# Performance work log

Measured on AMD Instinct MI355X. Metric: run time of the kernel, lower is better.

The kernel has to match this reference:

```python
import jax, jax.numpy as jnp
import numpy as np

H = 2048        # hidden_size
NH = 16         # num query heads
NKV = 4         # num kv heads
HD = 128        # head_dim
EPS = 1e-6
SCALE = HD ** -0.5
GROUPS = NH // NKV


def rotate_half(x):
    x1, x2 = x[..., : HD // 2], x[..., HD // 2:]
    return jnp.concatenate((-x2, x1), axis=-1)


def rmsnorm(x, w):
    # x: [..., HD]
    var = jnp.mean(jnp.square(x), axis=-1, keepdims=True)
    return x * jax.lax.rsqrt(var + EPS) * w


def setup_inputs() -> dict:
    key = jax.random.key(0)
    ks = jax.random.split(key, 10)
    B, QL, CL = 4, 1024, 3072
    s = 0.02
    return {
        "noise": jax.random.normal(ks[0], (B, QL, H), jnp.float32),
        "ctx": jax.random.normal(ks[1], (B, CL, H), jnp.float32),
        "cos": jax.random.uniform(ks[2], (B, CL + QL, HD), jnp.float32, -1.0, 1.0),
        "sin": jax.random.uniform(ks[3], (B, CL + QL, HD), jnp.float32, -1.0, 1.0),
        "Wq": jax.random.normal(ks[4], (H, NH * HD), jnp.float32) * s,
        "Wk": jax.random.normal(ks[5], (H, NKV * HD), jnp.float32) * s,
        "Wv": jax.random.normal(ks[6], (H, NKV * HD), jnp.float32) * s,
        "Wo": jax.random.normal(ks[7], (NH * HD, H), jnp.float32) * s,
        "qn_w": jnp.ones((HD,), jnp.float32),
        "kn_w": jnp.ones((HD,), jnp.float32),
    }


def reference(noise, ctx, cos, sin, Wq, Wk, Wv, Wo, qn_w, kn_w):
    B, QL, _ = noise.shape
    CL = ctx.shape[1]
    KL = CL + QL

    # Q from noise
    q = (noise @ Wq).reshape(B, QL, NH, HD)
    q = rmsnorm(q, qn_w).transpose(0, 2, 1, 3)            # [B, NH, QL, HD]

    # K/V from [ctx ; noise]
    kv_in = jnp.concatenate([ctx, noise], axis=1)          # [B, KL, H]
    k = (kv_in @ Wk).reshape(B, KL, NKV, HD)
    k = rmsnorm(k, kn_w).transpose(0, 2, 1, 3)             # [B, NKV, KL, HD]
    v = (kv_in @ Wv).reshape(B, KL, NKV, HD).transpose(0, 2, 1, 3)

    # RoPE: queries use last QL positions
    cos_q, sin_q = cos[:, -QL:, None].transpose(0, 2, 1, 3), sin[:, -QL:, None].transpose(0, 2, 1, 3)
    cos_k, sin_k = cos[:, None], sin[:, None]
    q = q * cos_q + rotate_half(q) * sin_q
    k = k * cos_k + rotate_half(k) * sin_k

    # GQA expansion
    k = jnp.repeat(k, GROUPS, axis=1)                      # [B, NH, KL, HD]
    v = jnp.repeat(v, GROUPS, axis=1)

    attn = jnp.einsum('bhqd,bhkd->bhqk', q, k) * SCALE     # [B, NH, QL, KL]
    attn = jax.nn.softmax(attn.astype(jnp.float32), axis=-1).astype(v.dtype)
    out = jnp.einsum('bhqk,bhkd->bhqd', attn, v)
    out = out.transpose(0, 2, 1, 3).reshape(B, QL, NH * HD)
    return out @ Wo
```

## Files before the change

kernel.cpp:

```cpp
#include <hip/hip_runtime.h>
#include <cstdint>
#include <cstddef>

#define DEVI __device__ __forceinline__

typedef short bf16x8 __attribute__((ext_vector_type(8)));
typedef short bf16x4 __attribute__((ext_vector_type(4)));
typedef float f32x4  __attribute__((ext_vector_type(4)));

constexpr int H_  = 2048;
constexpr int NH  = 16;
constexpr int NKV = 4;
constexpr int HD  = 128;
constexpr int B_  = 4;
constexpr int QL  = 1024;
constexpr int CL  = 3072;
constexpr int KL  = 4096;
constexpr float EPS = 1e-6f;
constexpr float SCALE_LOG2E = 0.08838834764831845f * 1.4426950408889634f;

DEVI unsigned short f2bf(float x) {
  unsigned int u = __float_as_uint(x);
  u += 0x7FFFu + ((u >> 16) & 1u);
  return (unsigned short)(u >> 16);
}
DEVI float bf2f(unsigned short u) {
  return __uint_as_float(((unsigned int)u) << 16);
}
DEVI bf16x4 mk4(float a, float b, float c, float d) {
  unsigned ua = __float_as_uint(a) + 0x8000u, ub = __float_as_uint(b) + 0x8000u;
  unsigned uc = __float_as_uint(c) + 0x8000u, ud = __float_as_uint(d) + 0x8000u;
  union { unsigned u[2]; bf16x4 v; } r;
  r.u[0] = __builtin_amdgcn_perm(ub, ua, 0x07060302u);
  r.u[1] = __builtin_amdgcn_perm(ud, uc, 0x07060302u);
  return r.v;
}

DEVI void async16(const void* g, void* l) {
  __builtin_amdgcn_global_load_lds(
      (const __attribute__((address_space(1))) void*)g,
      (__attribute__((address_space(3))) void*)l, 16, 0, 0);
}

__global__ __launch_bounds__(256)
void prep(const float* __restrict__ noise, const float* __restrict__ ctx,
          unsigned short* __restrict__ kvin) {
  const size_t t = (size_t)blockIdx.x * 256 + threadIdx.x;
  const size_t e = t * 8;
  const int row = (int)(e / H_), col = (int)(e % H_);
  const int b = row >> 12, pos = row & 4095;
  const float* src = (pos < CL) ? ctx + ((size_t)(b * CL + pos)) * H_ + col
                                : noise + ((size_t)(b * QL + (pos - CL))) * H_ + col;
  float4 x = ((const float4*)src)[0], y = ((const float4*)src)[1];
  bf16x8 v;
  v[0] = (short)f2bf(x.x); v[1] = (short)f2bf(x.y);
  v[2] = (short)f2bf(x.z); v[3] = (short)f2bf(x.w);
  v[4] = (short)f2bf(y.x); v[5] = (short)f2bf(y.y);
  v[6] = (short)f2bf(y.z); v[7] = (short)f2bf(y.w);
  *(bf16x8*)(kvin + e) = v;
}

__global__ __launch_bounds__(256)
void wtrans(const float* __restrict__ in, unsigned short* __restrict__ out,
            int K, int N) {
  __shared__ float t[64][65];
  const int ktiles = K >> 6;
  const int kt = blockIdx.x % ktiles;
  const int nt = blockIdx.x / ktiles;
  {
    const int r = threadIdx.x >> 2, cs = threadIdx.x & 3;
    const float4* src = (const float4*)(in + (size_t)(kt * 64 + r) * N + nt * 64 + cs * 16);
    #pragma unroll
    for (int i = 0; i < 4; ++i) {
      float4 v = src[i];
      t[r][cs * 16 + i * 4 + 0] = v.x;
      t[r][cs * 16 + i * 4 + 1] = v.y;
      t[r][cs * 16 + i * 4 + 2] = v.z;
      t[r][cs * 16 + i * 4 + 3] = v.w;
    }
  }
  __syncthreads();
  {
    const int n = threadIdx.x >> 2, ks = threadIdx.x & 3;
    bf16x8 o0, o1;
    #pragma unroll
    for (int i = 0; i < 8; ++i) o0[i] = (short)f2bf(t[ks * 16 + i][n]);
    #pragma unroll
    for (int i = 0; i < 8; ++i) o1[i] = (short)f2bf(t[ks * 16 + 8 + i][n]);
    unsigned short* op = out + (size_t)(nt * 64 + n) * K + kt * 64 + ks * 16;
    *(bf16x8*)(op) = o0;
    *(bf16x8*)(op + 8) = o1;
  }
}

template <int MODE>
__global__ __launch_bounds__(256)
void gemm2(const unsigned short* __restrict__ Abf,
           const unsigned short* __restrict__ Bt,
           const float* __restrict__ normw,
           const float* __restrict__ cosb, const float* __restrict__ sinb,
           unsigned short* __restrict__ outb, float* __restrict__ outf) {
  constexpr int M  = (MODE == 1 || MODE == 2) ? (B_ * KL) : (B_ * QL);
  constexpr int K  = H_;
  constexpr int MT = M / 128;

  __shared__ union U {
    struct { unsigned short a[128][64]; unsigned short b[128][64]; } st;
    unsigned short ct[128][138];
  } sm;

  const int tid  = threadIdx.x;
  const int tm   = blockIdx.x % MT;
  const int tn   = blockIdx.x / MT;
  const int wid  = tid >> 6, lane = tid & 63, quad = lane >> 4, lm = lane & 15;
  const int wm   = wid >> 1, wn = wid & 1;

  f32x4 acc[4][4];
  #pragma unroll
  for (int i = 0; i < 4; ++i)
    #pragma unroll
    for (int j = 0; j < 4; ++j)
      #pragma unroll
      for (int r = 0; r < 4; ++r) acc[i][j][r] = 0.f;

  const unsigned short* agp[4];
  const unsigned short* bgp[4];
  #pragma unroll
  for (int i = 0; i < 4; ++i) {
    const int idx = i * 256 + tid;
    const int arow = idx >> 3, g = idx & 7, gg = g ^ (arow & 7);
    int grow;
    if constexpr (MODE == 0) {
      const int gmr = tm * 128 + arow;
      grow = (gmr >> 10) * KL + CL + (gmr & 1023);
    } else {
      grow = tm * 128 + arow;
    }
    agp[i] = Abf + (size_t)grow * K + gg * 8;
    bgp[i] = Bt + (size_t)(tn * 128 + arow) * K + gg * 8;
  }

  for (int kt = 0; kt < K / 64; ++kt) {
    __syncthreads();
    #pragma unroll
    for (int i = 0; i < 4; ++i) {
      async16(agp[i] + kt * 64, (char*)&sm.st.a[0][0] + (i * 256 + wid * 64) * 16);
      async16(bgp[i] + kt * 64, (char*)&sm.st.b[0][0] + (i * 256 + wid * 64) * 16);
    }
    __syncthreads();
    #pragma unroll
    for (int ks = 0; ks < 2; ++ks) {
      bf16x8 af[4], bfr[4];
      #pragma unroll
      for (int i = 0; i < 4; ++i) {
        const int swz = (ks * 4 + quad) ^ (lm & 7);
        af[i] = *(const bf16x8*)&sm.st.a[wm * 64 + i * 16 + lm][swz * 8];
      }
      #pragma unroll
      for (int j = 0; j < 4; ++j) {
        const int swz = (ks * 4 + quad) ^ (lm & 7);
        bfr[j] = *(const bf16x8*)&sm.st.b[wn * 64 + j * 16 + lm][swz * 8];
      }
      #pragma unroll
      for (int i = 0; i < 4; ++i)
        #pragma unroll
        for (int j = 0; j < 4; ++j)
          acc[i][j] = __builtin_amdgcn_mfma_f32_16x16x32_bf16(af[i], bfr[j], acc[i][j], 0, 0, 0);
    }
  }

  if constexpr (MODE == 3) {
    #pragma unroll
    for (int i = 0; i < 4; ++i)
      #pragma unroll
      for (int j = 0; j < 4; ++j) {
        const int row = tm * 128 + wm * 64 + i * 16 + quad * 4;
        const int col = tn * 128 + wn * 64 + j * 16 + lm;
        #pragma unroll
        for (int rr = 0; rr < 4; ++rr)
          outf[(size_t)(row + rr) * H_ + col] = acc[i][j][rr];
      }
    return;
  }

  __syncthreads();
  #pragma unroll
  for (int i = 0; i < 4; ++i)
    #pragma unroll
    for (int j = 0; j < 4; ++j)
      #pragma unroll
      for (int rr = 0; rr < 4; ++rr)
        sm.ct[wm * 64 + i * 16 + quad * 4 + rr][wn * 64 + j * 16 + lm] =
            f2bf(acc[i][j][rr]);
  __syncthreads();

  const int row2 = tid >> 1, half = tid & 1;
  if constexpr (MODE == 0 || MODE == 1) {
    const int gmr = tm * 128 + row2;
    int ci; size_t obase;
    if constexpr (MODE == 0) {
      const int b = gmr >> 10, pos = gmr & 1023;
      ci = (b * KL + CL + pos) * HD;
      obase = ((size_t)((b * NH + tn) * QL + pos)) * HD;
    } else {
      const int b = gmr >> 12, pos = gmr & 4095;
      ci = (b * KL + pos) * HD;
      obase = ((size_t)((b * NKV + tn) * KL + pos)) * HD;
    }
    float ss = 0.f;
    for (int d = half * 64; d < half * 64 + 64; ++d) {
      float v = bf2f(sm.ct[row2][d]);
      ss += v * v;
    }
    ss += __shfl_xor(ss, 1);
    const float rinv = rsqrtf(ss * (1.0f / 128.0f) + EPS);
    constexpr float OSC = (MODE == 0) ? SCALE_LOG2E : 1.0f;
    #pragma unroll
    for (int d8 = 0; d8 < 8; ++d8) {
      bf16x8 v;
      #pragma unroll
      for (int j = 0; j < 8; ++j) {
        const int d = half * 64 + d8 * 8 + j;
        const float x  = bf2f(sm.ct[row2][d])      * rinv * normw[d];
        const float xo = bf2f(sm.ct[row2][d ^ 64]) * rinv * normw[d ^ 64];
        const float rot = (d < 64) ? -xo : xo;
        v[j] = (short)f2bf((x * cosb[ci + d] + rot * sinb[ci + d]) * OSC);
      }
      *(bf16x8*)(outb + obase + half * 64 + d8 * 8) = v;
    }
  } else {
    const int d = row2;
    const int b = (tm * 128) >> 12;
    const int posBase = ((tm * 128) & 4095) + half * 64;
    const size_t obase = ((size_t)((b * NKV + tn) * HD + d)) * KL + posBase;
    #pragma unroll
    for (int k8 = 0; k8 < 8; ++k8) {
      bf16x8 v;
      #pragma unroll
      for (int j = 0; j < 8; ++j)
        v[j] = (short)sm.ct[half * 64 + k8 * 8 + j][d];
      *(bf16x8*)(outb + obase + k8 * 8) = v;
    }
  }
}

__global__ __launch_bounds__(256)
void attn2(const unsigned short* __restrict__ qb,
           const unsigned short* __restrict__ kb,
           const unsigned short* __restrict__ vtb,
           unsigned short* __restrict__ ao) {
  __shared__ unsigned short kl[64][128];
  __shared__ unsigned short vl[128][64];

  const int tid = threadIdx.x;
  const int wave = tid >> 6, lane = tid & 63, quad = lane >> 4, lm = lane & 15;
  const int qblk = blockIdx.x & 7;
  const int bh = blockIdx.x >> 3;
  const int b = bh >> 4, h = bh & 15, kvh = h >> 2;
  const int q0 = qblk * 128 + wave * 32;

  bf16x8 qf[2][4];
  const unsigned short* qbase = qb + ((size_t)((b * NH + h) * QL + q0)) * HD;
  #pragma unroll
  for (int qt = 0; qt < 2; ++qt)
    #pragma unroll
    for (int kq = 0; kq < 4; ++kq)
      qf[qt][kq] = *(const bf16x8*)(qbase + (qt * 16 + lm) * HD + kq * 32 + quad * 8);

  f32x4 o[2][8];
  float li[2] = {0.f, 0.f};
  #pragma unroll
  for (int qt = 0; qt < 2; ++qt)
    #pragma unroll
    for (int dt = 0; dt < 8; ++dt)
      #pragma unroll
      for (int rr = 0; rr < 4; ++rr) o[qt][dt][rr] = 0.f;

  const unsigned short* kbase = kb + ((size_t)(b * NKV + kvh)) * KL * HD;
  const unsigned short* vbase = vtb + ((size_t)(b * NKV + kvh)) * HD * KL;

  const unsigned short* kgp[4];
  const unsigned short* vgp[4];
  #pragma unroll
  for (int i = 0; i < 4; ++i) {
    const int idx = i * 256 + tid;
    const int krow = idx >> 4, gc = idx & 15;
    const int gg = (gc & 8) | ((gc & 7) ^ (krow & 7));
    kgp[i] = kbase + (size_t)krow * HD + gg * 8;
    const int vrow = idx >> 3, g = idx & 7;
    const int gv = g ^ (vrow & 7);
    vgp[i] = vbase + (size_t)vrow * KL + gv * 8;
  }

  for (int kt = 0; kt < KL / 64; ++kt) {
    __syncthreads();
    #pragma unroll
    for (int i = 0; i < 4; ++i) {
      async16(kgp[i] + (size_t)kt * 64 * HD, (char*)&kl[0][0] + (i * 256 + wave * 64) * 16);
      async16(vgp[i] + kt * 64,              (char*)&vl[0][0] + (i * 256 + wave * 64) * 16);
    }
    __syncthreads();

    #pragma unroll
    for (int nt = 0; nt < 4; ++nt) {
      bf16x8 kf[4];
      #pragma unroll
      for (int kq = 0; kq < 4; ++kq) {
        const int gc = kq * 4 + quad;
        const int swz = (gc & 8) | ((gc & 7) ^ (lm & 7));
        kf[kq] = *(const bf16x8*)&kl[nt * 16 + lm][swz * 8];
      }
      f32x4 s0 = {0.f, 0.f, 0.f, 0.f}, s1 = {0.f, 0.f, 0.f, 0.f};
      #pragma unroll
      for (int kq = 0; kq < 4; ++kq) {
        s0 = __builtin_amdgcn_mfma_f32_16x16x32_bf16(kf[kq], qf[0][kq], s0, 0, 0, 0);
        s1 = __builtin_amdgcn_mfma_f32_16x16x32_bf16(kf[kq], qf[1][kq], s1, 0, 0, 0);
      }
      float e00 = __builtin_amdgcn_exp2f(s0[0]), e01 = __builtin_amdgcn_exp2f(s0[1]);
      float e02 = __builtin_amdgcn_exp2f(s0[2]), e03 = __builtin_amdgcn_exp2f(s0[3]);
      float e10 = __builtin_amdgcn_exp2f(s1[0]), e11 = __builtin_amdgcn_exp2f(s1[1]);
      float e12 = __builtin_amdgcn_exp2f(s1[2]), e13 = __builtin_amdgcn_exp2f(s1[3]);
      li[0] += (e00 + e01) + (e02 + e03);
      li[1] += (e10 + e11) + (e12 + e13);
      bf16x4 p0 = mk4(e00, e01, e02, e03);
      bf16x4 p1 = mk4(e10, e11, e12, e13);
      #pragma unroll
      for (int dt = 0; dt < 8; ++dt) {
        const int gv = (nt * 2 + (quad >> 1)) ^ (lm & 7);
        bf16x4 vf = *(const bf16x4*)&vl[dt * 16 + lm][gv * 8 + (quad & 1) * 4];
        o[0][dt] = __builtin_amdgcn_mfma_f32_16x16x16bf16_1k(vf, p0, o[0][dt], 0, 0, 0);
        o[1][dt] = __builtin_amdgcn_mfma_f32_16x16x16bf16_1k(vf, p1, o[1][dt], 0, 0, 0);
      }
    }
  }

  #pragma unroll
  for (int qt = 0; qt < 2; ++qt) {
    float l = li[qt];
    l += __shfl_xor(l, 16);
    l += __shfl_xor(l, 32);
    const float inv = 1.0f / l;
    const size_t rowbase = ((size_t)(b * QL + q0 + qt * 16 + lm)) * (NH * HD) + h * HD;
    #pragma unroll
    for (int dt = 0; dt < 8; ++dt) {
      bf16x4 v = mk4(o[qt][dt][0] * inv, o[qt][dt][1] * inv,
                     o[qt][dt][2] * inv, o[qt][dt][3] * inv);
      *(bf16x4*)(ao + rowbase + dt * 16 + quad * 4) = v;
    }
  }
}

extern "C" void kernel_launch(void* const* d_in, const int* in_sizes, int n_in,
                              void* d_out, int out_size, void* d_ws, size_t ws_size,
                              hipStream_t stream) {
  const float* noise = (const float*)d_in[0];
  const float* ctx   = (const float*)d_in[1];
  const float* cosb  = (const float*)d_in[2];
  const float* sinb  = (const float*)d_in[3];
  const float* Wq    = (const float*)d_in[4];
  const float* Wk    = (const float*)d_in[5];
  const float* Wv    = (const float*)d_in[6];
  const float* Wo    = (const float*)d_in[7];
  const float* qn    = (const float*)d_in[8];
  const float* kn    = (const float*)d_in[9];
  float* out = (float*)d_out;

  char* ws = (char*)d_ws;
  unsigned short* kvin = (unsigned short*)(ws);
  unsigned short* aob  = (unsigned short*)(ws);
  unsigned short* WqT  = (unsigned short*)(ws + 67108864);
  unsigned short* WkT  = (unsigned short*)(ws + 67108864 + 8388608);
  unsigned short* WvT  = (unsigned short*)(ws + 67108864 + 10485760);
  unsigned short* WoT  = (unsigned short*)(ws + 67108864 + 12582912);
  unsigned short* qbuf = (unsigned short*)(ws + 67108864 + 20971520);
  unsigned short* kbuf = (unsigned short*)(ws + 67108864 + 37748736);
  unsigned short* vtb  = (unsigned short*)(ws + 67108864 + 54525952);

  prep<<<dim3((B_ * KL * H_) / 8 / 256), dim3(256), 0, stream>>>(noise, ctx, kvin);

  wtrans<<<dim3(1024), dim3(256), 0, stream>>>(Wq, WqT, 2048, 2048);
  wtrans<<<dim3(256),  dim3(256), 0, stream>>>(Wk, WkT, 2048, 512);
  wtrans<<<dim3(256),  dim3(256), 0, stream>>>(Wv, WvT, 2048, 512);
  wtrans<<<dim3(1024), dim3(256), 0, stream>>>(Wo, WoT, 2048, 2048);

  gemm2<0><<<dim3(32 * 16), dim3(256), 0, stream>>>(
      kvin, WqT, qn, cosb, sinb, qbuf, nullptr);
  gemm2<1><<<dim3(128 * 4), dim3(256), 0, stream>>>(
      kvin, WkT, kn, cosb, sinb, kbuf, nullptr);
  gemm2<2><<<dim3(128 * 4), dim3(256), 0, stream>>>(
      kvin, WvT, nullptr, nullptr, nullptr, vtb, nullptr);

  attn2<<<dim3(512), dim3(256), 0, stream>>>(qbuf, kbuf, vtb, aob);

  gemm2<3><<<dim3(32 * 16), dim3(256), 0, stream>>>(
      aob, WoT, nullptr, nullptr, nullptr, nullptr, out);
}
```

Measured before the change: 617.8 us.

## Merge K/V projections, shrink GEMM row tiles, restructure attention to split keys across waves

The K and V projection GEMMs become one launch over a concatenated transposed weight, with column tiles beyond the K heads writing transposed V. The Q and output GEMMs use 64-row tiles, doubling the block count for better occupancy on a large-CU GPU, and the RoPE/norm epilogue now uses vectorized loads. Attention is rewritten so each block handles 64 queries and each wave handles 16 keys per step. Waves exchange probabilities through LDS and read K and V straight from global memory instead of staging them in LDS. This adds extra barriers per key tile and uncached-style global reads of K/V that may cost bandwidth.

```diff
diff --git a/kernel.cpp b/kernel.cpp
--- a/kernel.cpp
+++ b/kernel.cpp
@@ -93,20 +93,23 @@
   }
 }
 
-template <int MODE>
+template <int MODE, int BM>
 __global__ __launch_bounds__(256)
-void gemm2(const unsigned short* __restrict__ Abf,
+void gemm3(const unsigned short* __restrict__ Abf,
            const unsigned short* __restrict__ Bt,
            const float* __restrict__ normw,
            const float* __restrict__ cosb, const float* __restrict__ sinb,
-           unsigned short* __restrict__ outb, float* __restrict__ outf) {
-  constexpr int M  = (MODE == 1 || MODE == 2) ? (B_ * KL) : (B_ * QL);
+           unsigned short* __restrict__ outb, unsigned short* __restrict__ outb2,
+           float* __restrict__ outf) {
+  constexpr int M  = (MODE == 1) ? (B_ * KL) : (B_ * QL);
   constexpr int K  = H_;
-  constexpr int MT = M / 128;
-
-  __shared__ union U {
-    struct { unsigned short a[128][64]; unsigned short b[128][64]; } st;
-    unsigned short ct[128][138];
+  constexpr int MT = M / BM;
+  constexpr int WI = BM / 32;
+  constexpr int AG = BM * 8 / 256;
+
+  __shared__ union {
+    struct { unsigned short a[BM][64]; unsigned short b[128][64]; } st;
+    unsigned short ct[BM][138];
   } sm;
 
   const int tid  = threadIdx.x;
@@ -115,54 +118,57 @@
   const int wid  = tid >> 6, lane = tid & 63, quad = lane >> 4, lm = lane & 15;
   const int wm   = wid >> 1, wn = wid & 1;
 
-  f32x4 acc[4][4];
-  #pragma unroll
-  for (int i = 0; i < 4; ++i)
+  f32x4 acc[WI][4];
+  #pragma unroll
+  for (int i = 0; i < WI; ++i)
     #pragma unroll
     for (int j = 0; j < 4; ++j)
       #pragma unroll
       for (int r = 0; r < 4; ++r) acc[i][j][r] = 0.f;
 
-  const unsigned short* agp[4];
+  const unsigned short* agp[AG];
   const unsigned short* bgp[4];
   #pragma unroll
-  for (int i = 0; i < 4; ++i) {
+  for (int i = 0; i < AG; ++i) {
     const int idx = i * 256 + tid;
     const int arow = idx >> 3, g = idx & 7, gg = g ^ (arow & 7);
     int grow;
     if constexpr (MODE == 0) {
-      const int gmr = tm * 128 + arow;
+      const int gmr = tm * BM + arow;
       grow = (gmr >> 10) * KL + CL + (gmr & 1023);
     } else {
-      grow = tm * 128 + arow;
+      grow = tm * BM + arow;
     }
     agp[i] = Abf + (size_t)grow * K + gg * 8;
-    bgp[i] = Bt + (size_t)(tn * 128 + arow) * K + gg * 8;
+  }
+  #pragma unroll
+  for (int i = 0; i < 4; ++i) {
+    const int idx = i * 256 + tid;
+    const int brow = idx >> 3, g = idx & 7, gg = g ^ (brow & 7);
+    bgp[i] = Bt + (size_t)(tn * 128 + brow) * K + gg * 8;
   }
 
   for (int kt = 0; kt < K / 64; ++kt) {
     __syncthreads();
     #pragma unroll
-    for (int i = 0; i < 4; ++i) {
+    for (int i = 0; i < AG; ++i)
       async16(agp[i] + kt * 64, (char*)&sm.st.a[0][0] + (i * 256 + wid * 64) * 16);
+    #pragma unroll
+    for (int i = 0; i < 4; ++i)
       async16(bgp[i] + kt * 64, (char*)&sm.st.b[0][0] + (i * 256 + wid * 64) * 16);
-    }
     __syncthreads();
     #pragma unroll
     for (int ks = 0; ks < 2; ++ks) {
-      bf16x8 af[4], bfr[4];
-      #pragma unroll
-      for (int i = 0; i < 4; ++i) {
-        const int swz = (ks * 4 + quad) ^ (lm & 7);
-        af[i] = *(const bf16x8*)&sm.st.a[wm * 64 + i * 16 + lm][swz * 8];
-      }
-      #pragma unroll
-      for (int j = 0; j < 4; ++j) {
-        const int swz = (ks * 4 + quad) ^ (lm & 7);
+      const int swz = (ks * 4 + quad) ^ (lm & 7);
+      bf16x8 af[WI], bfr[4];
+      #pragma unroll
+      for (int i = 0; i < WI; ++i)
+        af[i] = *(const bf16x8*)&sm.st.a[wm * (BM / 2) + i * 16 + lm][swz * 8];
+      #pragma unroll
+      for (int j = 0; j < 4; ++j)
         bfr[j] = *(const bf16x8*)&sm.st.b[wn * 64 + j * 16 + lm][swz * 8];
-      }
-      #pragma unroll
-      for (int i = 0; i < 4; ++i)
+      #pragma unroll
+      for (int i = 0; i < WI; ++i)
         #pragma unroll
         for (int j = 0; j < 4; ++j)
           acc[i][j] = __builtin_amdgcn_mfma_f32_16x16x32_bf16(af[i], bfr[j], acc[i][j], 0, 0, 0);
@@ -171,10 +177,10 @@
 
   if constexpr (MODE == 3) {
     #pragma unroll
-    for (int i = 0; i < 4; ++i)
+    for (int i = 0; i < WI; ++i)
       #pragma unroll
       for (int j = 0; j < 4; ++j) {
-        const int row = tm * 128 + wm * 64 + i * 16 + quad * 4;
+        const int row = tm * BM + wm * (BM / 2) + i * 16 + quad * 4;
         const int col = tn * 128 + wn * 64 + j * 16 + lm;
         #pragma unroll
         for (int rr = 0; rr < 4; ++rr)
@@ -185,18 +191,39 @@
 
   __syncthreads();
   #pragma unroll
-  for (int i = 0; i < 4; ++i)
+  for (int i = 0; i < WI; ++i)
     #pragma unroll
     for (int j = 0; j < 4; ++j)
       #pragma unroll
       for (int rr = 0; rr < 4; ++rr)
-        sm.ct[wm * 64 + i * 16 + quad * 4 + rr][wn * 64 + j * 16 + lm] =
+        sm.ct[wm * (BM / 2) + i * 16 + quad * 4 + rr][wn * 64 + j * 16 + lm] =
             f2bf(acc[i][j][rr]);
   __syncthreads();
 
-  const int row2 = tid >> 1, half = tid & 1;
-  if constexpr (MODE == 0 || MODE == 1) {
-    const int gmr = tm * 128 + row2;
+  if constexpr (MODE == 1) {
+    if (tn >= 4) {
+      const int row2 = tid >> 1, half = tid & 1;
+      const int d = row2;
+      const int b = (tm * 128) >> 12;
+      const int posBase = ((tm * 128) & 4095) + half * 64;
+      const size_t obase = ((size_t)((b * NKV + (tn - 4)) * HD + d)) * KL + posBase;
+      #pragma unroll
+      for (int k8 = 0; k8 < 8; ++k8) {
+        bf16x8 v;
+        #pragma unroll
+        for (int j = 0; j < 8; ++j)
+          v[j] = (short)sm.ct[half * 64 + k8 * 8 + j][d];
+        *(bf16x8*)(outb2 + obase + k8 * 8) = v;
+      }
+      return;
+    }
+  }
+
+  {
+    constexpr int TPR = 256 / BM;
+    constexpr int SEG = 128 / TPR;
+    const int row2 = tid / TPR, part = tid % TPR;
+    const int gmr = tm * BM + row2;
     int ci; size_t obase;
     if constexpr (MODE == 0) {
       const int b = gmr >> 10, pos = gmr & 1023;
@@ -208,144 +235,154 @@
       obase = ((size_t)((b * NKV + tn) * KL + pos)) * HD;
     }
     float ss = 0.f;
-    for (int d = half * 64; d < half * 64 + 64; ++d) {
-      float v = bf2f(sm.ct[row2][d]);
-      ss += v * v;
-    }
-    ss += __shfl_xor(ss, 1);
+    #pragma unroll
+    for (int d8 = 0; d8 < SEG / 8; ++d8) {
+      bf16x8 v = *(const bf16x8*)&sm.ct[row2][part * SEG + d8 * 8];
+      #pragma unroll
+      for (int j = 0; j < 8; ++j) {
+        float x = bf2f((unsigned short)v[j]);
+        ss += x * x;
+      }
+    }
+    #pragma unroll
+    for (int off = 1; off < TPR; off <<= 1) ss += __shfl_xor(ss, off);
     const float rinv = rsqrtf(ss * (1.0f / 128.0f) + EPS);
     constexpr float OSC = (MODE == 0) ? SCALE_LOG2E : 1.0f;
     #pragma unroll
-    for (int d8 = 0; d8 < 8; ++d8) {
-      bf16x8 v;
+    for (int d8 = 0; d8 < SEG / 8; ++d8) {
+      const int dbase = part * SEG + d8 * 8;
+      bf16x8 v  = *(const bf16x8*)&sm.ct[row2][dbase];
+      bf16x8 mv = *(const bf16x8*)&sm.ct[row2][dbase ^ 64];
+      const float4 c0 = *(const float4*)&cosb[ci + dbase];
+      const float4 c1 = *(const float4*)&cosb[ci + dbase + 4];
+      const float4 s0 = *(const float4*)&sinb[ci + dbase];
+      const float4 s1 = *(const float4*)&sinb[ci + dbase + 4];
+      const float cs[8] = {c0.x, c0.y, c0.z, c0.w, c1.x, c1.y, c1.z, c1.w};
+      const float sn[8] = {s0.x, s0.y, s0.z, s0.w, s1.x, s1.y, s1.z, s1.w};
+      bf16x8 ov;
       #pragma unroll
       for (int j = 0; j < 8; ++j) {
-        const int d = half * 64 + d8 * 8 + j;
-        const float x  = bf2f(sm.ct[row2][d])      * rinv * normw[d];
-        const float xo = bf2f(sm.ct[row2][d ^ 64]) * rinv * normw[d ^ 64];
+        const int d = dbase + j;
+        const float x  = bf2f((unsigned short)v[j])  * rinv * normw[d];
+        const float xo = bf2f((unsigned short)mv[j]) * rinv * normw[d ^ 64];
         const float rot = (d < 64) ? -xo : xo;
-        v[j] = (short)f2bf((x * cosb[ci + d] + rot * sinb[ci + d]) * OSC);
+        ov[j] = (short)f2bf((x * cs[j] + rot * sn[j]) * OSC);
       }
-      *(bf16x8*)(outb + obase + half * 64 + d8 * 8) = v;
-    }
-  } else {
-    const int d = row2;
-    const int b = (tm * 128) >> 12;
-    const int posBase = ((tm * 128) & 4095) + half * 64;
-    const size_t obase = ((size_t)((b * NKV + tn) * HD + d)) * KL + posBase;
-    #pragma unroll
-    for (int k8 = 0; k8 < 8; ++k8) {
-      bf16x8 v;
-      #pragma unroll
-      for (int j = 0; j < 8; ++j)
-        v[j] = (short)sm.ct[half * 64 + k8 * 8 + j][d];
-      *(bf16x8*)(outb + obase + k8 * 8) = v;
+      *(bf16x8*)(outb + obase + dbase) = ov;
     }
   }
 }
 
 __global__ __launch_bounds__(256)
-void attn2(const unsigned short* __restrict__ qb,
+void attn3(const unsigned short* __restrict__ qb,
            const unsigned short* __restrict__ kb,
            const unsigned short* __restrict__ vtb,
            unsigned short* __restrict__ ao) {
-  __shared__ unsigned short kl[64][128];
-  __shared__ unsigned short vl[128][64];
+  __shared__ unsigned short Pl[64][64];
+  __shared__ float liw[4][64];
 
   const int tid = threadIdx.x;
-  const int wave = tid >> 6, lane = tid & 63, quad = lane >> 4, lm = lane & 15;
-  const int qblk = blockIdx.x & 7;
-  const int bh = blockIdx.x >> 3;
+  const int w = tid >> 6, lane = tid & 63, quad = lane >> 4, lm = lane & 15;
+  const int qblk = blockIdx.x & 15;
+  const int bh = blockIdx.x >> 4;
   const int b = bh >> 4, h = bh & 15, kvh = h >> 2;
-  const int q0 = qblk * 128 + wave * 32;
-
-  bf16x8 qf[2][4];
+  const int q0 = qblk * 64;
+
+  bf16x8 qf[4][4];
   const unsigned short* qbase = qb + ((size_t)((b * NH + h) * QL + q0)) * HD;
   #pragma unroll
-  for (int qt = 0; qt < 2; ++qt)
+  for (int qt = 0; qt < 4; ++qt)
     #pragma unroll
     for (int kq = 0; kq < 4; ++kq)
       qf[qt][kq] = *(const bf16x8*)(qbase + (qt * 16 + lm) * HD + kq * 32 + quad * 8);
 
-  f32x4 o[2][8];
-  float li[2] = {0.f, 0.f};
-  #pragma unroll
-  for (int qt = 0; qt < 2; ++qt)
-    #pragma unroll
-    for (int dt = 0; dt < 8; ++dt)
-      #pragma unroll
-      for (int rr = 0; rr < 4; ++rr) o[qt][dt][rr] = 0.f;
+  f32x4 o[2][4];
+  float liacc[4];
+  #pragma unroll
+  for (int dt = 0; dt < 2; ++dt)
+    #pragma unroll
+    for (int qt = 0; qt < 4; ++qt)
+      #pragma unroll
+      for (int rr = 0; rr < 4; ++rr) o[dt][qt][rr] = 0.f;
+  #pragma unroll
+  for (int qt = 0; qt < 4; ++qt) liacc[qt] = 0.f;
 
   const unsigned short* kbase = kb + ((size_t)(b * NKV + kvh)) * KL * HD;
   const unsigned short* vbase = vtb + ((size_t)(b * NKV + kvh)) * HD * KL;
 
-  const unsigned short* kgp[4];
-  const unsigned short* vgp[4];
-  #pragma unroll
-  for (int i = 0; i < 4; ++i) {
-    const int idx = i * 256 + tid;
-    const int krow = idx >> 4, gc = idx & 15;
-    const int gg = (gc & 8) | ((gc & 7) ^ (krow & 7));
-    kgp[i] = kbase + (size_t)krow * HD + gg * 8;
-    const int vrow = idx >> 3, g = idx & 7;
-    const int gv = g ^ (vrow & 7);
-    vgp[i] = vbase + (size_t)vrow * KL + gv * 8;
-  }
-
   for (int kt = 0; kt < KL / 64; ++kt) {
+    const int ktp = kt * 64;
+    bf16x8 kf[4];
+    const unsigned short* krow = kbase + (size_t)(ktp + w * 16 + lm) * HD;
+    #pragma unroll
+    for (int kq = 0; kq < 4; ++kq)
+      kf[kq] = *(const bf16x8*)(krow + kq * 32 + quad * 8);
+    f32x4 s[4];
+    #pragma unroll
+    for (int qt = 0; qt < 4; ++qt)
+      #pragma unroll
+      for (int rr = 0; rr < 4; ++rr) s[qt][rr] = 0.f;
+    #pragma unroll
+    for (int kq = 0; kq < 4; ++kq)
+      #pragma unroll
+      for (int qt = 0; qt < 4; ++qt)
+        s[qt] = __builtin_amdgcn_mfma_f32_16x16x32_bf16(kf[kq], qf[qt][kq], s[qt], 0, 0, 0);
+
+    bf16x4 pk[4];
+    #pragma unroll
+    for (int qt = 0; qt < 4; ++qt) {
+      float e0 = __builtin_amdgcn_exp2f(s[qt][0]);
+      float e1 = __builtin_amdgcn_exp2f(s[qt][1]);
+      float e2 = __builtin_amdgcn_exp2f(s[qt][2]);
+      float e3 = __builtin_amdgcn_exp2f(s[qt][3]);
+      liacc[qt] += (e0 + e1) + (e2 + e3);
+      pk[qt] = mk4(e0, e1, e2, e3);
+    }
+
     __syncthreads();
-    #pragma unroll
-    for (int i = 0; i < 4; ++i) {
-      async16(kgp[i] + (size_t)kt * 64 * HD, (char*)&kl[0][0] + (i * 256 + wave * 64) * 16);
-      async16(vgp[i] + kt * 64,              (char*)&vl[0][0] + (i * 256 + wave * 64) * 16);
-    }
+    const int wcol = (((w * 2 + (quad >> 1)) ^ (lm & 7)) << 3) + (quad & 1) * 4;
+    #pragma unroll
+    for (int qt = 0; qt < 4; ++qt)
+      *(bf16x4*)&Pl[qt * 16 + lm][wcol] = pk[qt];
     __syncthreads();
 
     #pragma unroll
-    for (int nt = 0; nt < 4; ++nt) {
-      bf16x8 kf[4];
-      #pragma unroll
-      for (int kq = 0; kq < 4; ++kq) {
-        const int gc = kq * 4 + quad;
-        const int swz = (gc & 8) | ((gc & 7) ^ (lm & 7));
-        kf[kq] = *(const bf16x8*)&kl[nt * 16 + lm][swz * 8];
+    for (int ch = 0; ch < 2; ++ch) {
+      bf16x8 vf[2];
+      #pragma unroll
+      for (int dt = 0; dt < 2; ++dt)
+        vf[dt] = *(const bf16x8*)(vbase + (size_t)(w * 32 + dt * 16 + lm) * KL +
+                                  ktp + ch * 32 + quad * 8);
+      #pragma unroll
+      for (int qt = 0; qt < 4; ++qt) {
+        const int rcol = ((ch * 4 + quad) ^ (lm & 7)) << 3;
+        bf16x8 pb = *(const bf16x8*)&Pl[qt * 16 + lm][rcol];
+        #pragma unroll
+        for (int dt = 0; dt < 2; ++dt)
+          o[dt][qt] = __builtin_amdgcn_mfma_f32_16x16x32_bf16(vf[dt], pb, o[dt][qt], 0, 0, 0);
       }
-      f32x4 s0 = {0.f, 0.f, 0.f, 0.f}, s1 = {0.f, 0.f, 0.f, 0.f};
-      #pragma unroll
-      for (int kq = 0; kq < 4; ++kq) {
-        s0 = __builtin_amdgcn_mfma_f32_16x16x32_bf16(kf[kq], qf[0][kq], s0, 0, 0, 0);
-        s1 = __builtin_amdgcn_mfma_f32_16x16x32_bf16(kf[kq], qf[1][kq], s1, 0, 0, 0);
-      }
-      float e00 = __builtin_amdgcn_exp2f(s0[0]), e01 = __builtin_amdgcn_exp2f(s0[1]);
-      float e02 = __builtin_amdgcn_exp2f(s0[2]), e03 = __builtin_amdgcn_exp2f(s0[3]);
-      float e10 = __builtin_amdgcn_exp2f(s1[0]), e11 = __builtin_amdgcn_exp2f(s1[1]);
-      float e12 = __builtin_amdgcn_exp2f(s1[2]), e13 = __builtin_amdgcn_exp2f(s1[3]);
-      li[0] += (e00 + e01) + (e02 + e03);
-      li[1] += (e10 + e11) + (e12 + e13);
-      bf16x4 p0 = mk4(e00, e01, e02, e03);
-      bf16x4 p1 = mk4(e10, e11, e12, e13);
-      #pragma unroll
-      for (int dt = 0; dt < 8; ++dt) {
-        const int gv = (nt * 2 + (quad >> 1)) ^ (lm & 7);
-        bf16x4 vf = *(const bf16x4*)&vl[dt * 16 + lm][gv * 8 + (quad & 1) * 4];
-        o[0][dt] = __builtin_amdgcn_mfma_f32_16x16x16bf16_1k(vf, p0, o[0][dt], 0, 0, 0);
-        o[1][dt] = __builtin_amdgcn_mfma_f32_16x16x16bf16_1k(vf, p1, o[1][dt], 0, 0, 0);
-      }
-    }
-  }
-
-  #pragma unroll
-  for (int qt = 0; qt < 2; ++qt) {
-    float l = li[qt];
-    l += __shfl_xor(l, 16);
-    l += __shfl_xor(l, 32);
+    }
+  }
+
+  #pragma unroll
+  for (int qt = 0; qt < 4; ++qt) {
+    float v = liacc[qt];
+    v += __shfl_xor(v, 16);
+    v += __shfl_xor(v, 32);
+    if (quad == 0) liw[w][qt * 16 + lm] = v;
+  }
+  __syncthreads();
+  #pragma unroll
+  for (int qt = 0; qt < 4; ++qt) {
+    const int q = qt * 16 + lm;
+    const float l = liw[0][q] + liw[1][q] + liw[2][q] + liw[3][q];
     const float inv = 1.0f / l;
-    const size_t rowbase = ((size_t)(b * QL + q0 + qt * 16 + lm)) * (NH * HD) + h * HD;
-    #pragma unroll
-    for (int dt = 0; dt < 8; ++dt) {
-      bf16x4 v = mk4(o[qt][dt][0] * inv, o[qt][dt][1] * inv,
-                     o[qt][dt][2] * inv, o[qt][dt][3] * inv);
-      *(bf16x4*)(ao + rowbase + dt * 16 + quad * 4) = v;
+    const size_t rowbase = ((size_t)(b * QL + q0 + q)) * (NH * HD) + h * HD;
+    #pragma unroll
+    for (int dt = 0; dt < 2; ++dt) {
+      bf16x4 vv = mk4(o[dt][qt][0] * inv, o[dt][qt][1] * inv,
+                      o[dt][qt][2] * inv, o[dt][qt][3] * inv);
+      *(bf16x4*)(ao + rowbase + w * 32 + dt * 16 + quad * 4) = vv;
     }
   }
 }
@@ -369,8 +406,7 @@
   unsigned short* kvin = (unsigned short*)(ws);
   unsigned short* aob  = (unsigned short*)(ws);
   unsigned short* WqT  = (unsigned short*)(ws + 67108864);
-  unsigned short* WkT  = (unsigned short*)(ws + 67108864 + 8388608);
-  unsigned short* WvT  = (unsigned short*)(ws + 67108864 + 10485760);
+  unsigned short* WkvT = (unsigned short*)(ws + 67108864 + 8388608);
   unsigned short* WoT  = (unsigned short*)(ws + 67108864 + 12582912);
   unsigned short* qbuf = (unsigned short*)(ws + 67108864 + 20971520);
   unsigned short* kbuf = (unsigned short*)(ws + 67108864 + 37748736);
@@ -379,19 +415,17 @@
   prep<<<dim3((B_ * KL * H_) / 8 / 256), dim3(256), 0, stream>>>(noise, ctx, kvin);
 
   wtrans<<<dim3(1024), dim3(256), 0, stream>>>(Wq, WqT, 2048, 2048);
-  wtrans<<<dim3(256),  dim3(256), 0, stream>>>(Wk, WkT, 2048, 512);
-  wtrans<<<dim3(256),  dim3(256), 0, stream>>>(Wv, WvT, 2048, 512);
+  wtrans<<<dim3(256),  dim3(256), 0, stream>>>(Wk, WkvT, 2048, 512);
+  wtrans<<<dim3(256),  dim3(256), 0, stream>>>(Wv, WkvT + (size_t)512 * 2048, 2048, 512);
   wtrans<<<dim3(1024), dim3(256), 0, stream>>>(Wo, WoT, 2048, 2048);
 
-  gemm2<0><<<dim3(32 * 16), dim3(256), 0, stream>>>(
-      kvin, WqT, qn, cosb, sinb, qbuf, nullptr);
-  gemm2<1><<<dim3(128 * 4), dim3(256), 0, stream>>>(
-      kvin, WkT, kn, cosb, sinb, kbuf, nullptr);
-  gemm2<2><<<dim3(128 * 4), dim3(256), 0, stream>>>(
-      kvin, WvT, nullptr, nullptr, nullptr, vtb, nullptr);
-
-  attn2<<<dim3(512), dim3(256), 0, stream>>>(qbuf, kbuf, vtb, aob);
-
-  gemm2<3><<<dim3(32 * 16), dim3(256), 0, stream>>>(
-      aob, WoT, nullptr, nullptr, nullptr, nullptr, out);
-}
+  gemm3<0, 64><<<dim3(64 * 16), dim3(256), 0, stream>>>(
+      kvin, WqT, qn, cosb, sinb, qbuf, nullptr, nullptr);
+  gemm3<1, 128><<<dim3(128 * 8), dim3(256), 0, stream>>>(
+      kvin, WkvT, kn, cosb, sinb, kbuf, vtb, nullptr);
+
+  attn3<<<dim3(1024), dim3(256), 0, stream>>>(qbuf, kbuf, vtb, aob);
+
+  gemm3<3, 64><<<dim3(64 * 16), dim3(256), 0, stream>>>(
+      aob, WoT, nullptr, nullptr, nullptr, nullptr, nullptr, out);
+}
```

Result: slower. 717.5 us (+16.1%).
